# Kernel tuning notes

Hardware: AMD Instinct MI355X
Metric: run time of the kernel (lower is better)

Reference implementation:

```python
import jax, jax.numpy as jnp
import numpy as np

THR = 0.6
EPS = 1e-12


def _mlp(x, w1, b1, w2, b2):
    # Linear -> ReLU -> (Dropout eval = identity) -> Linear
    return jax.nn.relu(x @ w1 + b1) @ w2 + b2


def setup_inputs() -> dict:
    B, H, D = 16384, 1024, 300
    key = jax.random.key(0)
    ks = jax.random.split(key, 32)
    s = 0.02
    inp = {
        'brics': jax.random.normal(ks[0], (B, H), jnp.float32),
        'function_group': jax.random.normal(ks[1], (B, H), jnp.float32),
        'pharmacophore': jax.random.normal(ks[2], (B, H), jnp.float32),
        # fingerprint encoders (brics / function_group / pharmacophore)
        'bw1': jax.random.normal(ks[3], (H, D), jnp.float32) * s,
        'bb1': jnp.zeros((D,), jnp.float32),
        'bw2': jax.random.normal(ks[4], (D, H), jnp.float32) * s,
        'bb2': jnp.zeros((H,), jnp.float32),
        'fw1': jax.random.normal(ks[5], (H, D), jnp.float32) * s,
        'fb1': jnp.zeros((D,), jnp.float32),
        'fw2': jax.random.normal(ks[6], (D, H), jnp.float32) * s,
        'fb2': jnp.zeros((H,), jnp.float32),
        'pw1': jax.random.normal(ks[7], (H, D), jnp.float32) * s,
        'pb1': jnp.zeros((D,), jnp.float32),
        'pw2': jax.random.normal(ks[8], (D, H), jnp.float32) * s,
        'pb2': jnp.zeros((H,), jnp.float32),
        # weight generator: Linear(3H, 3)
        'wg_W': jax.random.normal(ks[9], (3 * H, 3), jnp.float32) * s,
        'wg_b': jnp.zeros((3,), jnp.float32),
        # enhancement layer: Linear(H, H) + sigmoid
        'enh_W': jax.random.normal(ks[10], (H, H), jnp.float32) * s,
        'enh_b': jnp.zeros((H,), jnp.float32),
        # fusion layer: Linear(2H, H)
        'fus_W': jax.random.normal(ks[11], (2 * H, H), jnp.float32) * s,
        'fus_b': jnp.zeros((H,), jnp.float32),
    }
    return inp


def reference(brics, function_group, pharmacophore,
              bw1, bb1, bw2, bb2,
              fw1, fb1, fw2, fb2,
              pw1, pb1, pw2, pb2,
              wg_W, wg_b, enh_W, enh_b, fus_W, fus_b):
    B, H = brics.shape
    eb = _mlp(brics, bw1, bb1, bw2, bb2)            # [B,H]
    ef = _mlp(function_group, fw1, fb1, fw2, fb2)   # [B,H]
    ep = _mlp(pharmacophore, pw1, pb1, pw2, pb2)    # [B,H]

    E = jnp.stack([eb, ef, ep], axis=1)             # [B,3,H]
    En = E / jnp.maximum(jnp.linalg.norm(E, axis=-1, keepdims=True), EPS)

    # three unordered pairs (0,1),(0,2),(1,2); softmax-weighted sum is
    # permutation invariant, so the original python sort is a no-op.
    ii = jnp.array([0, 0, 1])
    jj = jnp.array([1, 2, 2])
    Ei, Ej = E[:, ii], E[:, jj]                     # [B,3,H]
    Eni, Enj = En[:, ii], En[:, jj]
    sim = jnp.sum(Eni * Enj, axis=-1)               # [B,3] cosine sims
    keep = sim > THR                                # pairs above threshold

    elem_mask = (Eni * Enj > THR).astype(E.dtype)   # [B,3,H]
    cf = 0.5 * (Ei + Ej) * elem_mask                # candidate common feats

    w = jax.nn.softmax(jnp.where(keep, sim, -1e9), axis=-1)  # [B,3]
    wsum = jnp.einsum('bp,bph->bh', w, cf)
    mean_fp = jnp.mean(E, axis=1)
    any_kept = jnp.any(keep, axis=-1, keepdims=True)
    common = jnp.where(any_kept, wsum, mean_fp)     # [B,H]

    all_cat = jnp.concatenate([eb, ef, ep], axis=1)          # [B,3H]
    fp_w = jax.nn.softmax(all_cat @ wg_W + wg_b, axis=1)     # [B,3]
    weighted_fp_sum = jnp.einsum('bk,bkh->bh', fp_w, E)

    enh = jax.nn.sigmoid(common @ enh_W + enh_b)
    enhanced_common = common * enh

    fused = jnp.concatenate([weighted_fp_sum, enhanced_common], axis=1) @ fus_W + fus_b
    return fused
```

## Files before the change

kernel.cpp:

```cpp
#include <hip/hip_runtime.h>
#include <stdint.h>


typedef __attribute__((ext_vector_type(8))) __bf16 bf16x8;
typedef __attribute__((ext_vector_type(8))) short short8;
typedef __attribute__((ext_vector_type(4))) float floatx4;

__device__ __forceinline__ uint16_t f2bf(float f) {
  union { float f; uint32_t u; } v; v.f = f;
  uint32_t r = v.u + 0x7fffu + ((v.u >> 16) & 1u);
  return (uint16_t)(r >> 16);
}
__device__ __forceinline__ float bf2f(uint16_t h) {
  union { uint32_t u; float f; } v; v.u = ((uint32_t)h) << 16;
  return v.f;
}
__device__ __forceinline__ void gload16(const void* g, void* l) {
  __builtin_amdgcn_global_load_lds(
      (const __attribute__((address_space(1))) void*)g,
      (__attribute__((address_space(3))) void*)l, 16, 0, 0);
}

__global__ void cfe_transpose3_cvt_kernel(const float* __restrict__ s0,
                                          const float* __restrict__ s1,
                                          const float* __restrict__ s2,
                                          uint16_t* __restrict__ dst, long dstStride,
                                          int K, int N, int Kpad, int Npad) {
  const float* src = (blockIdx.z == 0) ? s0 : ((blockIdx.z == 1) ? s1 : s2);
  uint16_t* d = dst + (long)blockIdx.z * dstStride;
  __shared__ float tile[32][33];
  const int tx = threadIdx.x & 31;
  const int ty = threadIdx.x >> 5;
  const int k0 = blockIdx.x * 32;
  const int n0 = blockIdx.y * 32;
#pragma unroll
  for (int i = 0; i < 4; i++) {
    int k = k0 + ty + 8 * i;
    int n = n0 + tx;
    tile[ty + 8 * i][tx] = (k < K && n < N) ? src[(long)k * N + n] : 0.f;
  }
  __syncthreads();
#pragma unroll
  for (int i = 0; i < 4; i++) {
    int n = n0 + ty + 8 * i;
    int k = k0 + tx;
    if (n < Npad && k < Kpad) d[(long)n * Kpad + k] = f2bf(tile[tx][ty + 8 * i]);
  }
}

template <int MODE, int AF32>
__global__ void cfe_gemm128(const void* __restrict__ A0, const void* __restrict__ A1,
                            const void* __restrict__ A2, int lda,
                            const uint16_t* __restrict__ Bt, long sBz, int ldb,
                            void* __restrict__ C, long sCz, int ldc, int colofs,
                            const float* __restrict__ bias0,
                            const float* __restrict__ bias1,
                            const float* __restrict__ bias2, int biasN,
                            const uint16_t* __restrict__ common, int K) {
  const int z = blockIdx.z;
  const void* Av = (z == 0) ? A0 : ((z == 1) ? A1 : A2);
  Bt += (long)z * sBz;
  const float* bias = (z == 0) ? bias0 : ((z == 1) ? bias1 : bias2);

  const int gx = gridDim.x;
  const int lin = blockIdx.y * gx + blockIdx.x;
  const int P = (gx * gridDim.y) >> 3;
  const int v = (lin & 7) * P + (lin >> 3);
  const long bm = (long)(v / gx) * 128;
  const long bn = (long)(v % gx) * 128;

  const int tid = threadIdx.x;
  const int wave = tid >> 6;
  const int lane = tid & 63;
  const int wm = wave >> 1;
  const int wn = wave & 1;

  __shared__ __attribute__((aligned(16))) uint16_t As[128 * 32];
  __shared__ __attribute__((aligned(16))) uint16_t Bs[128 * 32];

  floatx4 acc[4][4];
#pragma unroll
  for (int i = 0; i < 4; i++)
#pragma unroll
    for (int j = 0; j < 4; j++) acc[i][j] = (floatx4){0.f, 0.f, 0.f, 0.f};

  const int lrow = lane >> 2;
  const int lcol = (lane & 3) * 8;
  const uint16_t* Bp = Bt + (bn + wave * 32 + lrow) * (long)ldb + lcol;
  uint16_t* BsW0 = &Bs[(wave * 32) * 32];
  uint16_t* BsW1 = &Bs[(wave * 32 + 16) * 32];
  const uint16_t* Ap = nullptr;
  uint16_t* AsW0 = &As[(wave * 32) * 32];
  uint16_t* AsW1 = &As[(wave * 32 + 16) * 32];
  const float* ApF0 = nullptr;
  const float* ApF1 = nullptr;
  short8* AsF0 = (short8*)&As[(wave * 32 + lrow) * 32 + lcol];
  short8* AsF1 = (short8*)&As[(wave * 32 + 16 + lrow) * 32 + lcol];
  if constexpr (AF32) {
    ApF0 = (const float*)Av + (bm + wave * 32 + lrow) * (long)lda + lcol;
    ApF1 = ApF0 + 16 * (long)lda;
  } else {
    Ap = (const uint16_t*)Av + (bm + wave * 32 + lrow) * (long)lda + lcol;
  }

  const int fr = lane & 15;
  const int fq = lane >> 4;
  const uint16_t* ArBase = &As[(wm * 64 + fr) * 32 + fq * 8];
  const uint16_t* BrBase = &Bs[(wn * 64 + fr) * 32 + fq * 8];

  for (int k0 = 0; k0 < K; k0 += 32) {
    if constexpr (AF32) {
      float4 f0 = *(const float4*)(ApF0 + k0);
      float4 f1 = *(const float4*)(ApF0 + k0 + 4);
      float4 f2 = *(const float4*)(ApF1 + k0);
      float4 f3 = *(const float4*)(ApF1 + k0 + 4);
      gload16(Bp + k0, BsW0);
      gload16(Bp + 16 * (long)ldb + k0, BsW1);
      union { uint16_t u[8]; short8 s; } p0, p1;
      p0.u[0] = f2bf(f0.x); p0.u[1] = f2bf(f0.y); p0.u[2] = f2bf(f0.z); p0.u[3] = f2bf(f0.w);
      p0.u[4] = f2bf(f1.x); p0.u[5] = f2bf(f1.y); p0.u[6] = f2bf(f1.z); p0.u[7] = f2bf(f1.w);
      p1.u[0] = f2bf(f2.x); p1.u[1] = f2bf(f2.y); p1.u[2] = f2bf(f2.z); p1.u[3] = f2bf(f2.w);
      p1.u[4] = f2bf(f3.x); p1.u[5] = f2bf(f3.y); p1.u[6] = f2bf(f3.z); p1.u[7] = f2bf(f3.w);
      *AsF0 = p0.s;
      *AsF1 = p1.s;
    } else {
      gload16(Ap + k0, AsW0);
      gload16(Ap + 16 * (long)lda + k0, AsW1);
      gload16(Bp + k0, BsW0);
      gload16(Bp + 16 * (long)ldb + k0, BsW1);
    }
    __syncthreads();

    short8 a[4], b[4];
#pragma unroll
    for (int mi = 0; mi < 4; mi++) a[mi] = *(const short8*)(ArBase + mi * 16 * 32);
#pragma unroll
    for (int ni = 0; ni < 4; ni++) b[ni] = *(const short8*)(BrBase + ni * 16 * 32);
#pragma unroll
    for (int mi = 0; mi < 4; mi++)
#pragma unroll
      for (int ni = 0; ni < 4; ni++)
        acc[mi][ni] = __builtin_amdgcn_mfma_f32_16x16x32_bf16(
            __builtin_bit_cast(bf16x8, a[mi]), __builtin_bit_cast(bf16x8, b[ni]),
            acc[mi][ni], 0, 0, 0);
    __syncthreads();
  }

#pragma unroll
  for (int mi = 0; mi < 4; mi++) {
    long row = bm + wm * 64 + mi * 16 + fq * 4;
#pragma unroll
    for (int ni = 0; ni < 4; ni++) {
      long col = bn + wn * 64 + ni * 16 + fr;
      float bv = (col < biasN) ? bias[col] : 0.f;
#pragma unroll
      for (int r = 0; r < 4; r++) {
        float vv = acc[mi][ni][r] + bv;
        long idx = (row + r) * (long)ldc + colofs + col;
        if constexpr (MODE == 0) {
          ((uint16_t*)C)[(long)z * sCz + idx] = f2bf(fmaxf(vv, 0.f));
        } else if constexpr (MODE == 1) {
          ((uint16_t*)C)[(long)z * sCz + idx] = f2bf(vv);
        } else if constexpr (MODE == 2) {
          float c = bf2f(common[(row + r) * 1024 + col]);
          float s = 1.f / (1.f + __expf(-vv));
          ((uint16_t*)C)[idx] = f2bf(c * s);
        } else {
          ((float*)C)[idx] = vv;
        }
      }
    }
  }
}

__global__ void cfe_pointwise_kernel(const uint16_t* __restrict__ E,
                                     const float* __restrict__ wgW,
                                     const float* __restrict__ wgb,
                                     uint16_t* __restrict__ commonb,
                                     uint16_t* __restrict__ fusedA) {
  const int row = blockIdx.x;
  const int tid = threadIdx.x;
  const long ES = 16384L * 1024;
  const long base = (long)row * 1024 + tid * 4;

  ushort4 u0 = *(const ushort4*)(E + base);
  ushort4 u1 = *(const ushort4*)(E + ES + base);
  ushort4 u2 = *(const ushort4*)(E + 2 * ES + base);
  float eb[4] = {bf2f(u0.x), bf2f(u0.y), bf2f(u0.z), bf2f(u0.w)};
  float ef[4] = {bf2f(u1.x), bf2f(u1.y), bf2f(u1.z), bf2f(u1.w)};
  float ep[4] = {bf2f(u2.x), bf2f(u2.y), bf2f(u2.z), bf2f(u2.w)};

  float vals[9];
#pragma unroll
  for (int i = 0; i < 9; i++) vals[i] = 0.f;
#pragma unroll
  for (int j = 0; j < 4; j++) {
    int h = tid * 4 + j;
    vals[0] += eb[j] * eb[j];
    vals[1] += ef[j] * ef[j];
    vals[2] += ep[j] * ep[j];
    vals[3] += eb[j] * ef[j];
    vals[4] += eb[j] * ep[j];
    vals[5] += ef[j] * ep[j];
#pragma unroll
    for (int c = 0; c < 3; c++)
      vals[6 + c] += eb[j] * wgW[(long)h * 3 + c] +
                     ef[j] * wgW[(long)(1024 + h) * 3 + c] +
                     ep[j] * wgW[(long)(2048 + h) * 3 + c];
  }

#pragma unroll
  for (int i = 0; i < 9; i++) {
    float v = vals[i];
    for (int off = 32; off; off >>= 1) v += __shfl_down(v, off);
    vals[i] = v;
  }
  __shared__ float red[4][9];
  if ((tid & 63) == 0) {
#pragma unroll
    for (int i = 0; i < 9; i++) red[tid >> 6][i] = vals[i];
  }
  __syncthreads();
  float tot[9];
#pragma unroll
  for (int i = 0; i < 9; i++)
    tot[i] = red[0][i] + red[1][i] + red[2][i] + red[3][i];

  const float EPSF = 1e-12f;
  float nb = fmaxf(sqrtf(tot[0]), EPSF);
  float nf = fmaxf(sqrtf(tot[1]), EPSF);
  float np_ = fmaxf(sqrtf(tot[2]), EPSF);
  float s01 = tot[3] / (nb * nf);
  float s02 = tot[4] / (nb * np_);
  float s12 = tot[5] / (nf * np_);
  bool k01 = s01 > 0.6f, k02 = s02 > 0.6f, k12 = s12 > 0.6f;
  bool any = k01 | k02 | k12;
  float z0 = k01 ? s01 : -1e9f;
  float z1 = k02 ? s02 : -1e9f;
  float z2 = k12 ? s12 : -1e9f;
  float zm = fmaxf(z0, fmaxf(z1, z2));
  float w0 = __expf(z0 - zm), w1 = __expf(z1 - zm), w2 = __expf(z2 - zm);
  float wsum = w0 + w1 + w2;
  w0 /= wsum; w1 /= wsum; w2 /= wsum;

  float g0 = tot[6] + wgb[0], g1 = tot[7] + wgb[1], g2 = tot[8] + wgb[2];
  float gm = fmaxf(g0, fmaxf(g1, g2));
  float f0 = __expf(g0 - gm), f1 = __expf(g1 - gm), f2 = __expf(g2 - gm);
  float fs = f0 + f1 + f2;
  f0 /= fs; f1 /= fs; f2 /= fs;

  float inb = 1.f / nb, inf_ = 1.f / nf, inp = 1.f / np_;
  ushort4 co, wf;
  uint16_t cov[4], wfv[4];
#pragma unroll
  for (int j = 0; j < 4; j++) {
    float b = eb[j], f = ef[j], p = ep[j];
    float nbv = b * inb, nfv = f * inf_, npv = p * inp;
    float c01 = (nbv * nfv > 0.6f) ? 0.5f * (b + f) : 0.f;
    float c02 = (nbv * npv > 0.6f) ? 0.5f * (b + p) : 0.f;
    float c12 = (nfv * npv > 0.6f) ? 0.5f * (f + p) : 0.f;
    float ws = w0 * c01 + w1 * c02 + w2 * c12;
    float cm = any ? ws : (b + f + p) * (1.f / 3.f);
    float wfs = f0 * b + f1 * f + f2 * p;
    cov[j] = f2bf(cm);
    wfv[j] = f2bf(wfs);
  }
  co.x = cov[0]; co.y = cov[1]; co.z = cov[2]; co.w = cov[3];
  wf.x = wfv[0]; wf.y = wfv[1]; wf.z = wfv[2]; wf.w = wfv[3];
  *(ushort4*)(commonb + base) = co;
  *(ushort4*)(fusedA + (long)row * 2048 + tid * 4) = wf;
}

extern "C" void kernel_launch(void* const* d_in, const int* in_sizes, int n_in,
                              void* d_out, int out_size, void* d_ws, size_t ws_size,
                              hipStream_t stream) {
  (void)in_sizes; (void)n_in; (void)out_size; (void)ws_size;
  const float* brics = (const float*)d_in[0];
  const float* fg    = (const float*)d_in[1];
  const float* ph    = (const float*)d_in[2];
  const float* bw1 = (const float*)d_in[3];  const float* bb1 = (const float*)d_in[4];
  const float* bw2 = (const float*)d_in[5];  const float* bb2 = (const float*)d_in[6];
  const float* fw1 = (const float*)d_in[7];  const float* fb1 = (const float*)d_in[8];
  const float* fw2 = (const float*)d_in[9];  const float* fb2 = (const float*)d_in[10];
  const float* pw1 = (const float*)d_in[11]; const float* pb1 = (const float*)d_in[12];
  const float* pw2 = (const float*)d_in[13]; const float* pb2 = (const float*)d_in[14];
  const float* wgW = (const float*)d_in[15]; const float* wgb = (const float*)d_in[16];
  const float* enhW = (const float*)d_in[17]; const float* enhb = (const float*)d_in[18];
  const float* fusW = (const float*)d_in[19]; const float* fusb = (const float*)d_in[20];
  float* out = (float*)d_out;

  uint16_t* EB   = (uint16_t*)d_ws;
  uint16_t* FA   = EB + 3L * 16384 * 1024;
  uint16_t* W1T  = FA + 16384L * 2048;
  uint16_t* W2T  = W1T + 3L * 384 * 1024;
  uint16_t* ENHT = W2T + 3L * 1024 * 320;
  uint16_t* FUST = ENHT + 1024L * 1024;
  uint16_t* YB   = (uint16_t*)d_out;
  uint16_t* COM  = (uint16_t*)d_out;

  cfe_transpose3_cvt_kernel<<<dim3(32, 12, 3), 256, 0, stream>>>(
      bw1, fw1, pw1, W1T, 384L * 1024, 1024, 300, 1024, 384);
  cfe_transpose3_cvt_kernel<<<dim3(10, 32, 3), 256, 0, stream>>>(
      bw2, fw2, pw2, W2T, 1024L * 320, 300, 1024, 320, 1024);
  cfe_transpose3_cvt_kernel<<<dim3(32, 32, 1), 256, 0, stream>>>(
      enhW, enhW, enhW, ENHT, 0, 1024, 1024, 1024, 1024);
  cfe_transpose3_cvt_kernel<<<dim3(64, 32, 1), 256, 0, stream>>>(
      fusW, fusW, fusW, FUST, 0, 2048, 1024, 2048, 1024);

  cfe_gemm128<0, 1><<<dim3(3, 128, 3), 256, 0, stream>>>(
      brics, fg, ph, 1024, W1T, 384L * 1024, 1024,
      YB, 16384L * 384, 384, 0, bb1, fb1, pb1, 300, nullptr, 1024);

  cfe_gemm128<1, 0><<<dim3(8, 128, 3), 256, 0, stream>>>(
      YB, YB + 16384L * 384, YB + 2 * 16384L * 384, 384, W2T, 1024L * 320, 320,
      EB, 16384L * 1024, 1024, 0, bb2, fb2, pb2, 1024, nullptr, 320);

  cfe_pointwise_kernel<<<16384, 256, 0, stream>>>(EB, wgW, wgb, COM, FA);

  cfe_gemm128<2, 0><<<dim3(8, 128, 1), 256, 0, stream>>>(
      COM, COM, COM, 1024, ENHT, 0, 1024,
      FA, 0, 2048, 1024, enhb, enhb, enhb, 1024, COM, 1024);

  cfe_gemm128<3, 0><<<dim3(8, 128, 1), 256, 0, stream>>>(
      FA, FA, FA, 2048, FUST, 0, 2048,
      out, 0, 1024, 0, fusb, fusb, fusb, 1024, nullptr, 2048);
}
```

Measured before the change: 568.8 us.

## Prefetch fp32 A tiles, use native bf16 conversion, merge weight transposes

The fp32-input GEMM now loads the next k-step's A values into registers right after the barrier, so global load latency overlaps the MFMA work. The manual round-to-nearest bf16 conversion is replaced by the compiler's native __bf16 cast, which may map to hardware conversion instructions. The four weight transpose/convert launches are merged into one kernel that dispatches on block index, saving launch overhead. The prefetch raises register pressure, and the native cast could round differently on NaN edge cases.

```diff
diff --git a/kernel.cpp b/kernel.cpp
--- a/kernel.cpp
+++ b/kernel.cpp
@@ -7,13 +7,18 @@
 typedef __attribute__((ext_vector_type(4))) float floatx4;
 
 __device__ __forceinline__ uint16_t f2bf(float f) {
-  union { float f; uint32_t u; } v; v.f = f;
-  uint32_t r = v.u + 0x7fffu + ((v.u >> 16) & 1u);
-  return (uint16_t)(r >> 16);
+  __bf16 h = (__bf16)f;
+  return __builtin_bit_cast(uint16_t, h);
 }
 __device__ __forceinline__ float bf2f(uint16_t h) {
   union { uint32_t u; float f; } v; v.u = ((uint32_t)h) << 16;
   return v.f;
+}
+__device__ __forceinline__ short8 pack8(float4 a, float4 b) {
+  union { __bf16 h[8]; short8 s; } u;
+  u.h[0] = (__bf16)a.x; u.h[1] = (__bf16)a.y; u.h[2] = (__bf16)a.z; u.h[3] = (__bf16)a.w;
+  u.h[4] = (__bf16)b.x; u.h[5] = (__bf16)b.y; u.h[6] = (__bf16)b.z; u.h[7] = (__bf16)b.w;
+  return u.s;
 }
 __device__ __forceinline__ void gload16(const void* g, void* l) {
   __builtin_amdgcn_global_load_lds(
@@ -21,18 +26,34 @@
       (__attribute__((address_space(3))) void*)l, 16, 0, 0);
 }
 
-__global__ void cfe_transpose3_cvt_kernel(const float* __restrict__ s0,
-                                          const float* __restrict__ s1,
-                                          const float* __restrict__ s2,
-                                          uint16_t* __restrict__ dst, long dstStride,
-                                          int K, int N, int Kpad, int Npad) {
-  const float* src = (blockIdx.z == 0) ? s0 : ((blockIdx.z == 1) ? s1 : s2);
-  uint16_t* d = dst + (long)blockIdx.z * dstStride;
+__global__ void cfe_transpose_all(const float* __restrict__ bw1, const float* __restrict__ fw1,
+                                  const float* __restrict__ pw1, const float* __restrict__ bw2,
+                                  const float* __restrict__ fw2, const float* __restrict__ pw2,
+                                  const float* __restrict__ enhW, const float* __restrict__ fusW,
+                                  uint16_t* __restrict__ W1T, uint16_t* __restrict__ W2T,
+                                  uint16_t* __restrict__ ENHT, uint16_t* __restrict__ FUST) {
+  int bid = blockIdx.x;
+  const float* src; uint16_t* dst; int K, N, Kpad, Npad, bx, by;
+  if (bid < 1152) {
+    int z = bid / 384, t = bid % 384; bx = t % 32; by = t / 32;
+    src = (z == 0) ? bw1 : ((z == 1) ? fw1 : pw1); dst = W1T + (long)z * 384 * 1024;
+    K = 1024; N = 300; Kpad = 1024; Npad = 384;
+  } else if (bid < 2112) {
+    bid -= 1152; int z = bid / 320, t = bid % 320; bx = t % 10; by = t / 10;
+    src = (z == 0) ? bw2 : ((z == 1) ? fw2 : pw2); dst = W2T + (long)z * 1024 * 320;
+    K = 300; N = 1024; Kpad = 320; Npad = 1024;
+  } else if (bid < 3136) {
+    bid -= 2112; bx = bid % 32; by = bid / 32;
+    src = enhW; dst = ENHT; K = 1024; N = 1024; Kpad = 1024; Npad = 1024;
+  } else {
+    bid -= 3136; bx = bid % 64; by = bid / 64;
+    src = fusW; dst = FUST; K = 2048; N = 1024; Kpad = 2048; Npad = 1024;
+  }
   __shared__ float tile[32][33];
   const int tx = threadIdx.x & 31;
   const int ty = threadIdx.x >> 5;
-  const int k0 = blockIdx.x * 32;
-  const int n0 = blockIdx.y * 32;
+  const int k0 = bx * 32;
+  const int n0 = by * 32;
 #pragma unroll
   for (int i = 0; i < 4; i++) {
     int k = k0 + ty + 8 * i;
@@ -44,7 +65,7 @@
   for (int i = 0; i < 4; i++) {
     int n = n0 + ty + 8 * i;
     int k = k0 + tx;
-    if (n < Npad && k < Kpad) d[(long)n * Kpad + k] = f2bf(tile[tx][ty + 8 * i]);
+    if (n < Npad && k < Kpad) dst[(long)n * Kpad + k] = f2bf(tile[tx][ty + 8 * i]);
   }
 }
 
@@ -108,21 +129,20 @@
   const uint16_t* ArBase = &As[(wm * 64 + fr) * 32 + fq * 8];
   const uint16_t* BrBase = &Bs[(wn * 64 + fr) * 32 + fq * 8];
 
+  float4 f0, f1, f2, f3;
+  if constexpr (AF32) {
+    f0 = *(const float4*)(ApF0);
+    f1 = *(const float4*)(ApF0 + 4);
+    f2 = *(const float4*)(ApF1);
+    f3 = *(const float4*)(ApF1 + 4);
+  }
+
   for (int k0 = 0; k0 < K; k0 += 32) {
     if constexpr (AF32) {
-      float4 f0 = *(const float4*)(ApF0 + k0);
-      float4 f1 = *(const float4*)(ApF0 + k0 + 4);
-      float4 f2 = *(const float4*)(ApF1 + k0);
-      float4 f3 = *(const float4*)(ApF1 + k0 + 4);
       gload16(Bp + k0, BsW0);
       gload16(Bp + 16 * (long)ldb + k0, BsW1);
-      union { uint16_t u[8]; short8 s; } p0, p1;
-      p0.u[0] = f2bf(f0.x); p0.u[1] = f2bf(f0.y); p0.u[2] = f2bf(f0.z); p0.u[3] = f2bf(f0.w);
-      p0.u[4] = f2bf(f1.x); p0.u[5] = f2bf(f1.y); p0.u[6] = f2bf(f1.z); p0.u[7] = f2bf(f1.w);
-      p1.u[0] = f2bf(f2.x); p1.u[1] = f2bf(f2.y); p1.u[2] = f2bf(f2.z); p1.u[3] = f2bf(f2.w);
-      p1.u[4] = f2bf(f3.x); p1.u[5] = f2bf(f3.y); p1.u[6] = f2bf(f3.z); p1.u[7] = f2bf(f3.w);
-      *AsF0 = p0.s;
-      *AsF1 = p1.s;
+      *AsF0 = pack8(f0, f1);
+      *AsF1 = pack8(f2, f3);
     } else {
       gload16(Ap + k0, AsW0);
       gload16(Ap + 16 * (long)lda + k0, AsW1);
@@ -130,6 +150,15 @@
       gload16(Bp + 16 * (long)ldb + k0, BsW1);
     }
     __syncthreads();
+
+    if constexpr (AF32) {
+      if (k0 + 32 < K) {
+        f0 = *(const float4*)(ApF0 + k0 + 32);
+        f1 = *(const float4*)(ApF0 + k0 + 36);
+        f2 = *(const float4*)(ApF1 + k0 + 32);
+        f3 = *(const float4*)(ApF1 + k0 + 36);
+      }
+    }
 
     short8 a[4], b[4];
 #pragma unroll
@@ -298,14 +327,8 @@
   uint16_t* YB   = (uint16_t*)d_out;
   uint16_t* COM  = (uint16_t*)d_out;
 
-  cfe_transpose3_cvt_kernel<<<dim3(32, 12, 3), 256, 0, stream>>>(
-      bw1, fw1, pw1, W1T, 384L * 1024, 1024, 300, 1024, 384);
-  cfe_transpose3_cvt_kernel<<<dim3(10, 32, 3), 256, 0, stream>>>(
-      bw2, fw2, pw2, W2T, 1024L * 320, 300, 1024, 320, 1024);
-  cfe_transpose3_cvt_kernel<<<dim3(32, 32, 1), 256, 0, stream>>>(
-      enhW, enhW, enhW, ENHT, 0, 1024, 1024, 1024, 1024);
-  cfe_transpose3_cvt_kernel<<<dim3(64, 32, 1), 256, 0, stream>>>(
-      fusW, fusW, fusW, FUST, 0, 2048, 1024, 2048, 1024);
+  cfe_transpose_all<<<5184, 256, 0, stream>>>(
+      bw1, fw1, pw1, bw2, fw2, pw2, enhW, fusW, W1T, W2T, ENHT, FUST);
 
   cfe_gemm128<0, 1><<<dim3(3, 128, 3), 256, 0, stream>>>(
       brics, fg, ph, 1024, W1T, 384L * 1024, 1024,
```

New measurement: 544.6 us. -4.3%, faster.
